# Kernel tuning notes

Hardware: AMD Instinct MI355X
Metric: run time of the kernel (lower is better)

Reference implementation:

```python
import jax, jax.numpy as jnp
import numpy as np


def setup_inputs() -> dict:
    key = jax.random.key(0)
    k1, k2, k3, k4 = jax.random.split(key, 4)
    Na, Nb, Da, Db, S = 200000, 200000, 64, 64, 256
    a_locations = jax.random.randint(k1, (Na, 3), 0, S, dtype=jnp.int32)
    b_locations = jax.random.randint(k2, (Nb, 3), 0, S, dtype=jnp.int32)
    a_features = jax.random.normal(k3, (Na, Da), dtype=jnp.float32)
    b_features = jax.random.normal(k4, (Nb, Db), dtype=jnp.float32)
    return {
        "a_locations": a_locations,
        "a_features": a_features,
        "b_locations": b_locations,
        "b_features": b_features,
    }


def reference(a_locations, a_features, b_locations, b_features):
    # Stack all locations and dedup rows (torch.unique(dim=0, return_inverse=True)).
    # For jit-compatibility we use size=N (worst case: no duplicates) and pad
    # trailing unused rows with fill_value=-1 (features rows stay zero).
    locations = jnp.concatenate([a_locations, b_locations], axis=0)  # [N, 3]
    N = locations.shape[0]
    unique_locations, reverse_indices = jnp.unique(
        locations, axis=0, size=N, fill_value=-1, return_inverse=True
    )
    reverse_indices = reverse_indices.ravel()  # [N]

    Na, Da = a_features.shape
    Db = b_features.shape[1]
    a_rev = reverse_indices[:Na]
    b_rev = reverse_indices[Na:]

    # Scatter-concat: a goes into columns [:Da], b into columns [Da:].
    unique_features = jnp.zeros((N, Da + Db), dtype=a_features.dtype)
    unique_features = unique_features.at[a_rev, :Da].set(a_features)
    unique_features = unique_features.at[b_rev, Da:].set(b_features)
    return unique_locations, unique_features
```

## Files before the change

### kernel.cpp

```cpp
#include <hip/hip_runtime.h>
#include <hip/hip_bf16.h>

#define NKEYS   (1 << 24)
#define NBLK    16384
#define MAXN    400000

__device__ unsigned int g_counts[NKEYS];
__device__ unsigned int g_blockSums[NBLK];
__device__ int          g_winner_a[MAXN];
__device__ int          g_winner_b[MAXN];

__global__ void k_zero_counts() {
    int i = blockIdx.x * blockDim.x + threadIdx.x;
    reinterpret_cast<uint4*>(g_counts)[i] = make_uint4(0u, 0u, 0u, 0u);
}

__global__ void k_init(float* out_loc, int N) {
    int i = blockIdx.x * blockDim.x + threadIdx.x;
    if (i < N) { g_winner_a[i] = -1; g_winner_b[i] = -1; }
    if (i < N * 3) out_loc[i] = -1.0f;
}

__global__ void k_mark(const int* __restrict__ a_loc, const int* __restrict__ b_loc,
                       int Na, int N) {
    int i = blockIdx.x * blockDim.x + threadIdx.x;
    if (i >= N) return;
    const int* p = (i < Na) ? (a_loc + (size_t)i * 3) : (b_loc + (size_t)(i - Na) * 3);
    int key = (p[0] << 16) | (p[1] << 8) | p[2];
    g_counts[key] = 1u;
}

__global__ void k_block_reduce() {
    __shared__ unsigned int s[256];
    int b = blockIdx.x, t = threadIdx.x;
    uint4 c = *reinterpret_cast<const uint4*>(&g_counts[b * 1024 + t * 4]);
    s[t] = c.x + c.y + c.z + c.w;
    __syncthreads();
    for (int off = 128; off > 0; off >>= 1) {
        if (t < off) s[t] += s[t + off];
        __syncthreads();
    }
    if (t == 0) g_blockSums[b] = s[0];
}

__global__ void k_scan_blocks() {
    __shared__ unsigned int s[1024];
    int tid = threadIdx.x;
    int base = tid * 16;
    unsigned int local[16];
    unsigned int tot = 0;
#pragma unroll
    for (int k = 0; k < 16; ++k) { local[k] = g_blockSums[base + k]; tot += local[k]; }
    s[tid] = tot;
    __syncthreads();
    for (int off = 1; off < 1024; off <<= 1) {
        unsigned int v = (tid >= off) ? s[tid - off] : 0u;
        __syncthreads();
        s[tid] += v;
        __syncthreads();
    }
    unsigned int run = s[tid] - tot;
#pragma unroll
    for (int k = 0; k < 16; ++k) { unsigned int c = local[k]; g_blockSums[base + k] = run; run += c; }
}

__global__ void k_rank_write_loc(float* __restrict__ out_loc) {
    __shared__ unsigned int s[256];
    int b = blockIdx.x, t = threadIdx.x;
    int k0 = b * 1024 + t * 4;
    uint4 c = *reinterpret_cast<const uint4*>(&g_counts[k0]);
    unsigned int pres[4] = { c.x, c.y, c.z, c.w };
    unsigned int cnt = c.x + c.y + c.z + c.w;
    s[t] = cnt;
    __syncthreads();
    for (int off = 1; off < 256; off <<= 1) {
        unsigned int v = (t >= off) ? s[t - off] : 0u;
        __syncthreads();
        s[t] += v;
        __syncthreads();
    }
    unsigned int r = g_blockSums[b] + s[t] - cnt;
#pragma unroll
    for (int k = 0; k < 4; ++k) {
        if (pres[k]) {
            int key = k0 + k;
            g_counts[key] = r;
            float* p = out_loc + (size_t)r * 3;
            p[0] = (float)(key >> 16);
            p[1] = (float)((key >> 8) & 255);
            p[2] = (float)(key & 255);
            ++r;
        }
    }
}

__global__ void k_reverse(const int* __restrict__ a_loc, const int* __restrict__ b_loc,
                          int Na, int N) {
    int i = blockIdx.x * blockDim.x + threadIdx.x;
    if (i >= N) return;
    const int* p = (i < Na) ? (a_loc + (size_t)i * 3) : (b_loc + (size_t)(i - Na) * 3);
    int key = (p[0] << 16) | (p[1] << 8) | p[2];
    unsigned int r = g_counts[key];
    if (i < Na) atomicMax(&g_winner_a[r], i);
    else        atomicMax(&g_winner_b[r], i - Na);
}

__global__ void k_gather(const float* __restrict__ a_feat, const float* __restrict__ b_feat,
                         float* __restrict__ out_feat, int N) {
    int idx = blockIdx.x * blockDim.x + threadIdx.x;
    if (idx >= N * 32) return;
    int u  = idx >> 5;
    int c4 = (idx & 31) * 4;
    float4 v = make_float4(0.f, 0.f, 0.f, 0.f);
    if (c4 < 64) {
        int w = g_winner_a[u];
        if (w >= 0) v = *reinterpret_cast<const float4*>(a_feat + (size_t)w * 64 + c4);
    } else {
        int w = g_winner_b[u];
        if (w >= 0) v = *reinterpret_cast<const float4*>(b_feat + (size_t)w * 64 + (c4 - 64));
    }
    *reinterpret_cast<float4*>(out_feat + (size_t)u * 128 + c4) = v;
}

extern "C" void kernel_launch(void* const* d_in, const int* in_sizes, int n_in,
                              void* d_out, int out_size, void* d_ws, size_t ws_size,
                              hipStream_t stream) {
    const int*   a_loc  = (const int*)  d_in[0];
    const float* a_feat = (const float*)d_in[1];
    const int*   b_loc  = (const int*)  d_in[2];
    const float* b_feat = (const float*)d_in[3];

    const int Na = in_sizes[0] / 3;
    const int Nb = in_sizes[2] / 3;
    const int N  = Na + Nb;

    float* out_loc  = (float*)d_out;
    float* out_feat = out_loc + (size_t)N * 3;

    const int T = 256;

    k_zero_counts<<<NKEYS / 4 / T, T, 0, stream>>>();
    k_init<<<(N * 3 + T - 1) / T, T, 0, stream>>>(out_loc, N);
    k_mark<<<(N + T - 1) / T, T, 0, stream>>>(a_loc, b_loc, Na, N);
    k_block_reduce<<<NBLK, T, 0, stream>>>();
    k_scan_blocks<<<1, 1024, 0, stream>>>();
    k_rank_write_loc<<<NBLK, T, 0, stream>>>(out_loc);
    k_reverse<<<(N + T - 1) / T, T, 0, stream>>>(a_loc, b_loc, Na, N);
    k_gather<<<(N * 32 + T - 1) / T, T, 0, stream>>>(a_feat, b_feat, out_feat, N);
}
```

Before: 183.0 us.

## Replace dense count array with presence bitmap and popcount-based ranking

Swaps the 16M-entry uint32 presence/rank array for a 512K-word bitmap set with atomicOr, plus a per-word prefix array. Ranks are then recovered with popcount on the masked word. This cuts the zeroing, reduce and scan traffic over the key space by roughly 32x, and the separate zero kernel is folded into init. In exchange it adds atomic contention on shared bitmap words and a serial bit-iteration loop in the location writer.

```diff
diff --git a/kernel.cpp b/kernel.cpp
--- a/kernel.cpp
+++ b/kernel.cpp
@@ -2,21 +2,22 @@
 #include <hip/hip_bf16.h>
 
 #define NKEYS   (1 << 24)
-#define NBLK    16384
+#define NW      (NKEYS / 32)
+#define WPT     4
+#define TPB     256
+#define WPB     (TPB * WPT)
+#define NBLK2   (NW / WPB)
 #define MAXN    400000
 
-__device__ unsigned int g_counts[NKEYS];
-__device__ unsigned int g_blockSums[NBLK];
+__device__ unsigned int g_bits[NW];
+__device__ unsigned int g_wordPrefix[NW];
+__device__ unsigned int g_blockSums[NBLK2];
 __device__ int          g_winner_a[MAXN];
 __device__ int          g_winner_b[MAXN];
 
-__global__ void k_zero_counts() {
-    int i = blockIdx.x * blockDim.x + threadIdx.x;
-    reinterpret_cast<uint4*>(g_counts)[i] = make_uint4(0u, 0u, 0u, 0u);
-}
-
 __global__ void k_init(float* out_loc, int N) {
     int i = blockIdx.x * blockDim.x + threadIdx.x;
+    if (i < NW / 4) reinterpret_cast<uint4*>(g_bits)[i] = make_uint4(0u, 0u, 0u, 0u);
     if (i < N) { g_winner_a[i] = -1; g_winner_b[i] = -1; }
     if (i < N * 3) out_loc[i] = -1.0f;
 }
@@ -27,64 +28,61 @@
     if (i >= N) return;
     const int* p = (i < Na) ? (a_loc + (size_t)i * 3) : (b_loc + (size_t)(i - Na) * 3);
     int key = (p[0] << 16) | (p[1] << 8) | p[2];
-    g_counts[key] = 1u;
+    atomicOr(&g_bits[key >> 5], 1u << (key & 31));
 }
 
-__global__ void k_block_reduce() {
-    __shared__ unsigned int s[256];
+__global__ void k_reduce() {
+    __shared__ unsigned int s[TPB];
     int b = blockIdx.x, t = threadIdx.x;
-    uint4 c = *reinterpret_cast<const uint4*>(&g_counts[b * 1024 + t * 4]);
-    s[t] = c.x + c.y + c.z + c.w;
+    uint4 w = reinterpret_cast<const uint4*>(g_bits)[b * TPB + t];
+    s[t] = __popc(w.x) + __popc(w.y) + __popc(w.z) + __popc(w.w);
     __syncthreads();
-    for (int off = 128; off > 0; off >>= 1) {
+    for (int off = TPB / 2; off > 0; off >>= 1) {
         if (t < off) s[t] += s[t + off];
         __syncthreads();
     }
     if (t == 0) g_blockSums[b] = s[0];
 }
 
-__global__ void k_scan_blocks() {
-    __shared__ unsigned int s[1024];
-    int tid = threadIdx.x;
-    int base = tid * 16;
-    unsigned int local[16];
-    unsigned int tot = 0;
-#pragma unroll
-    for (int k = 0; k < 16; ++k) { local[k] = g_blockSums[base + k]; tot += local[k]; }
-    s[tid] = tot;
+__global__ void k_scan() {
+    __shared__ unsigned int s[NBLK2];
+    int t = threadIdx.x;
+    unsigned int v = g_blockSums[t];
+    s[t] = v;
     __syncthreads();
-    for (int off = 1; off < 1024; off <<= 1) {
-        unsigned int v = (tid >= off) ? s[tid - off] : 0u;
+    for (int off = 1; off < NBLK2; off <<= 1) {
+        unsigned int u = (t >= off) ? s[t - off] : 0u;
         __syncthreads();
-        s[tid] += v;
+        s[t] += u;
         __syncthreads();
     }
-    unsigned int run = s[tid] - tot;
-#pragma unroll
-    for (int k = 0; k < 16; ++k) { unsigned int c = local[k]; g_blockSums[base + k] = run; run += c; }
+    g_blockSums[t] = s[t] - v;
 }
 
-__global__ void k_rank_write_loc(float* __restrict__ out_loc) {
-    __shared__ unsigned int s[256];
+__global__ void k_prefix_loc(float* __restrict__ out_loc) {
+    __shared__ unsigned int s[TPB];
     int b = blockIdx.x, t = threadIdx.x;
-    int k0 = b * 1024 + t * 4;
-    uint4 c = *reinterpret_cast<const uint4*>(&g_counts[k0]);
-    unsigned int pres[4] = { c.x, c.y, c.z, c.w };
-    unsigned int cnt = c.x + c.y + c.z + c.w;
+    int w0 = (b * TPB + t) * WPT;
+    uint4 wv = reinterpret_cast<const uint4*>(g_bits)[b * TPB + t];
+    unsigned int wlocal[WPT] = { wv.x, wv.y, wv.z, wv.w };
+    unsigned int cnt = __popc(wv.x) + __popc(wv.y) + __popc(wv.z) + __popc(wv.w);
     s[t] = cnt;
     __syncthreads();
-    for (int off = 1; off < 256; off <<= 1) {
-        unsigned int v = (t >= off) ? s[t - off] : 0u;
+    for (int off = 1; off < TPB; off <<= 1) {
+        unsigned int u = (t >= off) ? s[t - off] : 0u;
         __syncthreads();
-        s[t] += v;
+        s[t] += u;
         __syncthreads();
     }
     unsigned int r = g_blockSums[b] + s[t] - cnt;
 #pragma unroll
-    for (int k = 0; k < 4; ++k) {
-        if (pres[k]) {
-            int key = k0 + k;
-            g_counts[key] = r;
+    for (int j = 0; j < WPT; ++j) {
+        unsigned int bits = wlocal[j];
+        g_wordPrefix[w0 + j] = r;
+        while (bits) {
+            int bit = __ffs(bits) - 1;
+            bits &= bits - 1;
+            int key = ((w0 + j) << 5) | bit;
             float* p = out_loc + (size_t)r * 3;
             p[0] = (float)(key >> 16);
             p[1] = (float)((key >> 8) & 255);
@@ -100,7 +98,8 @@
     if (i >= N) return;
     const int* p = (i < Na) ? (a_loc + (size_t)i * 3) : (b_loc + (size_t)(i - Na) * 3);
     int key = (p[0] << 16) | (p[1] << 8) | p[2];
-    unsigned int r = g_counts[key];
+    unsigned int word = g_bits[key >> 5];
+    unsigned int r = g_wordPrefix[key >> 5] + __popc(word & ((1u << (key & 31)) - 1u));
     if (i < Na) atomicMax(&g_winner_a[r], i);
     else        atomicMax(&g_winner_b[r], i - Na);
 }
@@ -137,14 +136,11 @@
     float* out_loc  = (float*)d_out;
     float* out_feat = out_loc + (size_t)N * 3;
 
-    const int T = 256;
-
-    k_zero_counts<<<NKEYS / 4 / T, T, 0, stream>>>();
-    k_init<<<(N * 3 + T - 1) / T, T, 0, stream>>>(out_loc, N);
-    k_mark<<<(N + T - 1) / T, T, 0, stream>>>(a_loc, b_loc, Na, N);
-    k_block_reduce<<<NBLK, T, 0, stream>>>();
-    k_scan_blocks<<<1, 1024, 0, stream>>>();
-    k_rank_write_loc<<<NBLK, T, 0, stream>>>(out_loc);
-    k_reverse<<<(N + T - 1) / T, T, 0, stream>>>(a_loc, b_loc, Na, N);
-    k_gather<<<(N * 32 + T - 1) / T, T, 0, stream>>>(a_feat, b_feat, out_feat, N);
+    k_init<<<(N * 3 + TPB - 1) / TPB, TPB, 0, stream>>>(out_loc, N);
+    k_mark<<<(N + TPB - 1) / TPB, TPB, 0, stream>>>(a_loc, b_loc, Na, N);
+    k_reduce<<<NBLK2, TPB, 0, stream>>>();
+    k_scan<<<1, NBLK2, 0, stream>>>();
+    k_prefix_loc<<<NBLK2, TPB, 0, stream>>>(out_loc);
+    k_reverse<<<(N + TPB - 1) / TPB, TPB, 0, stream>>>(a_loc, b_loc, Na, N);
+    k_gather<<<(N * 32 + TPB - 1) / TPB, TPB, 0, stream>>>(a_feat, b_feat, out_feat, N);
 }
```

Result: faster. 153.6 us (-16.0%).
